# Performance work log

Measured on AMD Instinct MI355X. Metric: run time of the kernel, lower is better.

Reference implementation:

```python
import jax, jax.numpy as jnp
import numpy as np

N = 8192       # num_nodes
DEG = 16       # edges per node
E = N * DEG    # num_edges
F = 128        # num_features
R = 20         # num_rbf_features
L = 3          # num_message_passing_layers
CUT = 3.0      # cutoff_dist


def setup_inputs() -> dict:
    key = jax.random.key(0)
    ks = jax.random.split(key, 18)
    atoms = jax.random.randint(ks[0], (N,), 1, 119)
    # every node appears as a destination exactly DEG times -> bincount > 0
    idx_i = jnp.repeat(jnp.arange(N), DEG)
    idx_j = jax.random.randint(ks[1], (E,), 0, N)
    raw = jax.random.normal(ks[2], (E, 3), jnp.float32)
    rel_dir = raw / jnp.linalg.norm(raw, axis=-1, keepdims=True)
    rel_dist = jax.random.uniform(ks[3], (E,), jnp.float32, 0.1, CUT - 1e-3)
    emb = (jax.random.normal(ks[4], (119, F), jnp.float32) / np.sqrt(F)).at[0].set(0.0)
    def w(k, shape, fan_in):
        return jax.random.normal(k, shape, jnp.float32) / np.sqrt(fan_in)
    return {
        'atoms': atoms, 'idx_i': idx_i, 'idx_j': idx_j,
        'rel_dir': rel_dir, 'rel_dist': rel_dist, 'emb': emb,
        'msg_w1': w(ks[5], (L, F, F), F), 'msg_b1': jnp.zeros((L, F), jnp.float32),
        'msg_w2': w(ks[6], (L, F, 3 * F), F), 'msg_b2': jnp.zeros((L, 3 * F), jnp.float32),
        'rbf_w': w(ks[7], (L, R, 3 * F), R), 'rbf_b': jnp.zeros((L, 3 * F), jnp.float32),
        'Uw': w(ks[8], (L, F, F), F), 'Vw': w(ks[9], (L, F, F), F),
        'upd_w1': w(ks[10], (L, 2 * F, F), 2 * F), 'upd_b1': jnp.zeros((L, F), jnp.float32),
        'upd_w2': w(ks[11], (L, F, 3 * F), F), 'upd_b2': jnp.zeros((L, 3 * F), jnp.float32),
    }


def painn_forward(atoms, idx_i, idx_j, rel_dir, rel_dist, emb,
                  msg_w1, msg_b1, msg_w2, msg_b2, rbf_w, rbf_b,
                  Uw, Vw, upd_w1, upd_b1, upd_w2, upd_b2):
    silu = jax.nn.silu
    # cosine cutoff and sinusoidal RBF features of edge distances
    cut = 0.5 * (jnp.cos(jnp.pi * rel_dist / CUT) + 1.0)               # [E]
    n = jnp.arange(1, R + 1, dtype=rel_dist.dtype)
    rbf = jnp.sin(n * jnp.pi * rel_dist[:, None] / CUT) / rel_dist[:, None]  # [E,R]

    s = emb[atoms]                                   # [N,F]
    v = jnp.zeros((N, F, 3), s.dtype)                # [N,F,3]
    counts = jax.ops.segment_sum(jnp.ones(E, s.dtype), idx_i, num_segments=N)  # bincount

    for l in range(L):
        # ---- message block ----
        phi = silu(s @ msg_w1[l] + msg_b1[l]) @ msg_w2[l] + msg_b2[l]  # [N,3F]
        W = (rbf @ rbf_w[l] + rbf_b[l]) * cut[:, None]                 # [E,3F]
        phi_W = phi[idx_j] * W                                         # [E,3F]
        p_vv, p_ss, p_vs = jnp.split(phi_W, 3, axis=-1)
        ds = jax.ops.segment_sum(p_ss, idx_i, num_segments=N) / counts[:, None]
        ve = v[idx_j] * p_vv[..., None] + p_vs[..., None] * rel_dir[:, None, :]  # [E,F,3]
        dv = jax.ops.segment_sum(ve, idx_i, num_segments=N) / counts[:, None, None]
        s = s + ds
        v = v + dv
        # ---- update block ----
        Uv = jnp.einsum('nfc,fg->ngc', v, Uw[l])       # [N,F,3]
        Vv = jnp.einsum('nfc,fg->ngc', v, Vw[l])       # [N,F,3]
        a_in = jnp.concatenate([jnp.linalg.norm(Vv, axis=-1), s], axis=-1)  # [N,2F]
        a = silu(a_in @ upd_w1[l] + upd_b1[l]) @ upd_w2[l] + upd_b2[l]      # [N,3F]
        a_vv, a_sv, a_ss = jnp.split(a, 3, axis=-1)
        s = s + a_ss + a_sv * jnp.sum(Uv * Vv, axis=-1)
        v = v + Uv * a_vv[..., None]
    return s, v


def reference(atoms, idx_i, idx_j, rel_dir, rel_dist, emb,
              msg_w1, msg_b1, msg_w2, msg_b2, rbf_w, rbf_b,
              Uw, Vw, upd_w1, upd_b1, upd_w2, upd_b2):
    return painn_forward(atoms, idx_i, idx_j, rel_dir, rel_dist, emb,
                         msg_w1, msg_b1, msg_w2, msg_b2, rbf_w, rbf_b,
                         Uw, Vw, upd_w1, upd_b1, upd_w2, upd_b2)
```

## Files before the change

### kernel.cpp

```cpp
#include <hip/hip_runtime.h>
#include <hip/hip_fp16.h>

#define N_NODES 8192
#define DEG     16
#define NEDGE   (N_NODES*DEG)
#define F       128
#define F3      384
#define RBF     20
#define NLAYER  3
#define NF      (N_NODES*F)
#define PI_F    3.14159265358979f

typedef unsigned short u16;
typedef __bf16 bf16x8 __attribute__((ext_vector_type(8)));
typedef float  f32x4  __attribute__((ext_vector_type(4)));
typedef _Float16 f16x2 __attribute__((ext_vector_type(2)));

__device__ __forceinline__ float bf2f(u16 u){ return __uint_as_float(((unsigned)u)<<16); }
__device__ __forceinline__ u16 f2bf(float f){
  unsigned x = __float_as_uint(f);
  unsigned r = (x + 0x7FFFu + ((x>>16)&1u)) >> 16;
  return (u16)r;
}
__device__ __forceinline__ float lo_bf(unsigned u){ return __uint_as_float(u<<16); }
__device__ __forceinline__ float hi_bf(unsigned u){ return __uint_as_float(u & 0xFFFF0000u); }
__device__ __forceinline__ float silu_f(float x){ return x / (1.f + __expf(-x)); }
__device__ __forceinline__ float ldsrc(const void* src, int i, int bf){
  return bf ? bf2f(((const u16*)src)[i]) : ((const float*)src)[i];
}
__device__ __forceinline__ unsigned packh2(float a, float b){
  return (unsigned)__half_as_ushort(__float2half(a)) |
         ((unsigned)__half_as_ushort(__float2half(b)) << 16);
}
__device__ __forceinline__ float fdot2u(unsigned a, unsigned b, float c){
  return __builtin_amdgcn_fdot2(__builtin_bit_cast(f16x2, a),
                                __builtin_bit_cast(f16x2, b), c, false);
}

__global__ void k_detect(const u16* __restrict__ rd, int* __restrict__ flag){
  if (threadIdx.x == 0 && blockIdx.x == 0){
    int ok = 1;
    for (int i = 0; i < 128; i++){
      float v = bf2f(rd[2*i]);
      if (!(v > 0.01f && v < 4.0f)) { ok = 0; break; }
    }
    *flag = ok;
  }
}

__device__ __forceinline__ void splitw(const void* src, u16* bh, u16* bl,
                                       int i, int K, int Ncol, int bf){
  int kn = K*Ncol; int l = i/kn; int r = i - l*kn; int k = r/Ncol; int n = r - k*Ncol;
  float w = ldsrc(src, i, bf);
  u16 h = f2bf(w);
  size_t o = (size_t)l*kn + (size_t)n*K + k;
  bh[o] = h; bl[o] = f2bf(w - bf2f(h));
}

__global__ __launch_bounds__(256) void k_prep(
    const void* mb1, const void* mb2, const void* b1, const void* b2,
    const void* rw,  const void* rb,
    const void* mw1, const void* mw2, const void* w1, const void* w2,
    const void* Uw,  const void* Vw,
    const void* dist, const void* dirv, const int* __restrict__ idxj,
    const int* __restrict__ atoms, const void* __restrict__ emb,
    float* c_mb1, float* c_mb2, float* c_b1, float* c_b2,
    unsigned* rwp2,
    u16* mw1h, u16* mw1l, u16* mw2h, u16* mw2l, u16* w1h, u16* w1l,
    u16* w2h, u16* w2l, u16* uvh, u16* uvl,
    uint4* edata,
    float* s, u16* s_h, u16* s_l,
    u16* p0h, u16* p0l, u16* bufA16, u16* bufB16,
    const int* __restrict__ flag){
  int i = blockIdx.x*256 + threadIdx.x;
  int bf = *flag;
  const int S0=NLAYER*F, S1=NLAYER*F3, S2=NLAYER*F, S3=NLAYER*F3;
  const int S4=NLAYER*11*F3;
  const int S5=NLAYER*F*F, S6=NLAYER*F*F3, S7=NLAYER*2*F*F, S8=NLAYER*F*F3, S9=NLAYER*256*F;
  if (i < S0){ c_mb1[i]=ldsrc(mb1,i,bf); return; } i-=S0;
  if (i < S1){ c_mb2[i]=ldsrc(mb2,i,bf); return; } i-=S1;
  if (i < S2){ c_b1[i] =ldsrc(b1, i,bf); return; } i-=S2;
  if (i < S3){ c_b2[i] =ldsrc(b2, i,bf); return; } i-=S3;
  if (i < S4){
    int l = i/(11*F3); int r = i - l*(11*F3); int r2 = r/F3; int col = r - r2*F3;
    float w0, w1v;
    if (r2 < 10){
      w0  = ldsrc(rw, (l*RBF + 2*r2  )*F3 + col, bf);
      w1v = ldsrc(rw, (l*RBF + 2*r2+1)*F3 + col, bf);
    } else {
      w0  = ldsrc(rb, l*F3 + col, bf);
      w1v = 0.f;
    }
    rwp2[i] = packh2(w0, w1v);
    return;
  } i-=S4;
  if (i < S5){ splitw(mw1, mw1h, mw1l, i, F,   F,  bf); return; } i-=S5;
  if (i < S6){ splitw(mw2, mw2h, mw2l, i, F,   F3, bf); return; } i-=S6;
  if (i < S7){ splitw(w1,  w1h,  w1l,  i, 2*F, F,  bf); return; } i-=S7;
  if (i < S8){ splitw(w2,  w2h,  w2l,  i, F,   F3, bf); return; } i-=S8;
  if (i < S9){
    int l=i/(256*F); int r=i-l*(256*F); int n=r>>7; int k=r&127;
    int si=(l*F+k)*F+(n&127);
    float w = ldsrc((n<128)?Uw:Vw, si, bf);
    u16 h=f2bf(w); uvh[i]=h; uvl[i]=f2bf(w-bf2f(h));
    return;
  } i-=S9;
  if (i < NEDGE){
    int e = i;
    float d = ldsrc(dist, e, bf);
    float th = PI_F*d*(1.f/3.f);
    float c  = __cosf(th);
    float s1 = __sinf(th);
    float cut = 0.5f*(c + 1.0f);
    float ic = cut/d;
    float sk[RBF+1];
    sk[0] = s1; float sm1 = 0.f, s0 = s1;
    #pragma unroll
    for (int k=1;k<=RBF;k++){ float sn = 2.f*c*s0 - sm1; sk[k-1] = s0; sm1 = s0; s0 = sn; }
    unsigned o[16];
    #pragma unroll
    for (int r2=0;r2<10;r2++)
      o[r2] = packh2(sk[2*r2]*ic, sk[2*r2+1]*ic);
    o[10] = packh2(cut, 0.f);
    o[11] = __float_as_uint(ldsrc(dirv, e*3+0, bf));
    o[12] = __float_as_uint(ldsrc(dirv, e*3+1, bf));
    o[13] = __float_as_uint(ldsrc(dirv, e*3+2, bf));
    o[14] = (unsigned)idxj[e];
    o[15] = 0;
    uint4* dst = edata + (size_t)e*4;
    dst[0] = make_uint4(o[0],o[1],o[2],o[3]);
    dst[1] = make_uint4(o[4],o[5],o[6],o[7]);
    dst[2] = make_uint4(o[8],o[9],o[10],o[11]);
    dst[3] = make_uint4(o[12],o[13],o[14],o[15]);
    return;
  } i-=NEDGE;
  if (i < NF){
    int n = i >> 7, f = i & 127;
    float sv = ldsrc(emb, atoms[n]*F + f, bf);
    s[i] = sv;
    u16 hb = f2bf(sv); s_h[i] = hb; s_l[i] = f2bf(sv - bf2f(hb));
    p0h[i]=0; p0h[NF+i]=0; p0h[2*(size_t)NF+i]=0;
    p0l[i]=0; p0l[NF+i]=0; p0l[2*(size_t)NF+i]=0;
    bufA16[(size_t)i*4+2]=0; bufA16[(size_t)i*4+3]=0;
    bufB16[(size_t)i*2+1]=0;
  }
}
#define PREP_TOTAL (NLAYER*(F+F3+F+F3+11*F3+F*F+F*F3+2*F*F+F*F3+256*F) + NEDGE + NF)

__global__ __launch_bounds__(256) void k_msg(const u16* __restrict__ s_h,
                                             const u16* __restrict__ s_l,
                                             const u16* __restrict__ w1h_,
                                             const u16* __restrict__ w1l_,
                                             const u16* __restrict__ w2h_,
                                             const u16* __restrict__ w2l_,
                                             const float* __restrict__ b1,
                                             const float* __restrict__ b2,
                                             u16* __restrict__ bufA16,
                                             u16* __restrict__ bufB16){
  __shared__ u16 Ah[16*136], Al[16*136];
  __shared__ u16 Hh[16*136], Hl[16*136];
  __shared__ u16 Bh[64*136], Bl[64*136];
  int t = threadIdx.x, lane = t&63, w = t>>6;
  int row0 = blockIdx.x<<4;
  int l15 = lane&15, q8 = (lane>>4)<<3, qrow = (lane>>4)<<2;

  #pragma unroll
  for (int q=0;q<2;q++){
    int id = t + 256*q; int pl = id>>8, rem = id&255, r = rem>>4, c = (rem&15)<<3;
    *(uint4*)((pl?Al:Ah)+r*136+c) = *(const uint4*)((pl?s_l:s_h) + (size_t)(row0+r)*F + c);
  }

  for (int cg=0;cg<2;cg++){
    __syncthreads();
    #pragma unroll
    for (int q=0;q<8;q++){
      int id = t + 256*q; int pl = id>>10, rem = id&1023, r = rem>>4, c = (rem&15)<<3;
      *(uint4*)((pl?Bl:Bh)+r*136+c) = *(const uint4*)((pl?w1l_:w1h_) + (size_t)(cg*64+r)*F + c);
    }
    __syncthreads();
    f32x4 acc; acc[0]=0;acc[1]=0;acc[2]=0;acc[3]=0;
// ... 21 lines not shown
  for (int cg=0;cg<6;cg++){
    __syncthreads();
    #pragma unroll
    for (int q=0;q<8;q++){
      int id = t + 256*q; int pl = id>>10, rem = id&1023, r = rem>>4, c = (rem&15)<<3;
      *(uint4*)((pl?Bl:Bh)+r*136+c) = *(const uint4*)((pl?w2l_:w2h_) + (size_t)(cg*64+r)*F + c);
    }
    __syncthreads();
    f32x4 acc; acc[0]=0;acc[1]=0;acc[2]=0;acc[3]=0;
    #pragma unroll
    for (int k0=0;k0<F;k0+=32){
      bf16x8 a_h = *(const bf16x8*)&Hh[l15*136 + k0 + q8];
      bf16x8 a_l = *(const bf16x8*)&Hl[l15*136 + k0 + q8];
      bf16x8 b_h = *(const bf16x8*)&Bh[(w*16+l15)*136 + k0 + q8];
      bf16x8 b_l = *(const bf16x8*)&Bl[(w*16+l15)*136 + k0 + q8];
      acc = __builtin_amdgcn_mfma_f32_16x16x32_bf16(a_h, b_h, acc, 0,0,0);
      acc = __builtin_amdgcn_mfma_f32_16x16x32_bf16(a_h, b_l, acc, 0,0,0);
      acc = __builtin_amdgcn_mfma_f32_16x16x32_bf16(a_l, b_h, acc, 0,0,0);
    }
    int gc = cg*64 + w*16 + l15;
    float bb = b2[gc];
    #pragma unroll
    for (int r=0;r<4;r++){
      int grow = row0 + qrow + r;
      u16 v = f2bf(acc[r] + bb);
      size_t rowo = (size_t)grow*F;
      if (gc < F)        bufA16[(rowo + gc)*4 + 0]     = v;
      else if (gc < 2*F) bufA16[(rowo + gc - F)*4 + 1] = v;
      else               bufB16[(rowo + gc - 2*F)*2]   = v;
    }
  }
}

__global__ __launch_bounds__(256) void k_agg(const uint4* __restrict__ ed_g,
                                             const uint2* __restrict__ bufA,
                                             const unsigned* __restrict__ bufB,
                                             const unsigned* __restrict__ rwp2,
                                             const u16* __restrict__ vi_h,
                                             const u16* __restrict__ vi_l,
                                             u16* __restrict__ vo_h,
                                             u16* __restrict__ vo_l,
                                             float* __restrict__ s,
                                             u16* __restrict__ s_h,
                                             u16* __restrict__ s_l){
  __shared__ uint4 ed4[128];
  int t = threadIdx.x;
  int half = t >> 7, f = t & 127;

  unsigned rw2[3][11];
  #pragma unroll
  for (int r2=0;r2<11;r2++){
    rw2[0][r2] = rwp2[r2*F3 + f];
    rw2[1][r2] = rwp2[r2*F3 + F + f];
    rw2[2][r2] = rwp2[r2*F3 + 2*F + f];
  }

  int nA = blockIdx.x * 2;
  if (t < 128) ed4[t] = ed_g[(size_t)nA*64 + t];
  __syncthreads();

  int n = nA + half;
  int base = half*64;
  float ds=0.f, dv0=0.f, dv1=0.f, dv2=0.f;

  int j0 = (int)(ed4[base+3].z & (N_NODES-1));
  uint2    pa = bufA[(size_t)j0*F + f];
  unsigned pb = bufB[(size_t)j0*F + f];
  for (int el=0;el<DEG;el++){
    uint2 cpa = pa; unsigned cpb = pb;
    if (el+1 < DEG){
      int j1 = (int)(ed4[base+(el+1)*4+3].z & (N_NODES-1));
      pa = bufA[(size_t)j1*F + f];
      pb = bufB[(size_t)j1*F + f];
    }
    uint4 q0 = ed4[base+el*4+0];
    uint4 q1 = ed4[base+el*4+1];
    uint4 q2 = ed4[base+el*4+2];
    uint4 q3 = ed4[base+el*4+3];
    unsigned rc[11] = {q0.x,q0.y,q0.z,q0.w, q1.x,q1.y,q1.z,q1.w, q2.x,q2.y,q2.z};
    float Wvv = 0.f, Wss = 0.f, Wvs = 0.f;
    #pragma unroll
    for (int r2=0;r2<11;r2++){
      Wvv = fdot2u(rc[r2], rw2[0][r2], Wvv);
      Wss = fdot2u(rc[r2], rw2[1][r2], Wss);
      Wvs = fdot2u(rc[r2], rw2[2][r2], Wvs);
    }
    float pvv = Wvv*lo_bf(cpa.x), pss = Wss*hi_bf(cpa.x), pvs = Wvs*lo_bf(cpb);
    ds += pss;
    dv0 += lo_bf(cpa.y)*pvv + pvs*__uint_as_float(q2.w);
    dv1 += hi_bf(cpa.y)*pvv + pvs*__uint_as_float(q3.x);
    dv2 += hi_bf(cpb)  *pvv + pvs*__uint_as_float(q3.y);
  }
  size_t i = (size_t)n*F + f;
  const float inv = 1.f/DEG;
  float sv = s[i] + ds*inv;
  s[i] = sv;
  { u16 hb = f2bf(sv); s_h[i] = hb; s_l[i] = f2bf(sv - bf2f(hb)); }
  float o0 = bf2f(vi_h[i])              + bf2f(vi_l[i])              + dv0*inv;
  float o1 = bf2f(vi_h[NF+i])           + bf2f(vi_l[NF+i])           + dv1*inv;
  float o2 = bf2f(vi_h[2*(size_t)NF+i]) + bf2f(vi_l[2*(size_t)NF+i]) + dv2*inv;
  u16 h0=f2bf(o0), h1=f2bf(o1), h2=f2bf(o2);
  vo_h[i]=h0; vo_h[NF+i]=h1; vo_h[2*(size_t)NF+i]=h2;
  vo_l[i]=f2bf(o0-bf2f(h0)); vo_l[NF+i]=f2bf(o1-bf2f(h1)); vo_l[2*(size_t)NF+i]=f2bf(o2-bf2f(h2));
}

struct Pre4 { uint4 v0, v1, v2, v3; };

__device__ __forceinline__ Pre4 load_tile(int idx, int t,
    const u16* uvh, const u16* uvl,
    const u16* w1h_, const u16* w1l_,
    const u16* w2h_, const u16* w2l_,
    const u16* mw1h_, const u16* mw1l_,
    const u16* mw2h_, const u16* mw2l_){
  const u16 *bh, *bl; int st, off;
  if (idx < 4){       bh=uvh;   bl=uvl;   st=128; off = idx*(64*128); }
  else if (idx < 8){  int r2=idx-4;
                      bh=w1h_;  bl=w1l_;  st=256; off = (r2&1)*(64*256) + (r2>>1)*128; }
  else if (idx < 14){ bh=w2h_;  bl=w2l_;  st=128; off = (idx-8)*(64*128); }
  else if (idx < 16){ bh=mw1h_; bl=mw1l_; st=128; off = (idx-14)*(64*128); }
  else {              bh=mw2h_; bl=mw2l_; st=128; off = (idx-16)*(64*128); }
  Pre4 p;
  { int id=t;      int hl=id>>10, rem=id&1023, r=rem>>4, c8=(rem&15)<<3;
    p.v0 = *(const uint4*)((hl?bl:bh) + (size_t)off + r*st + c8); }
  { int id=t+512;  int hl=id>>10, rem=id&1023, r=rem>>4, c8=(rem&15)<<3;
    p.v1 = *(const uint4*)((hl?bl:bh) + (size_t)off + r*st + c8); }
  { int id=t+1024; int hl=id>>10, rem=id&1023, r=rem>>4, c8=(rem&15)<<3;
    p.v2 = *(const uint4*)((hl?bl:bh) + (size_t)off + r*st + c8); }
  { int id=t+1536; int hl=id>>10, rem=id&1023, r=rem>>4, c8=(rem&15)<<3;
    p.v3 = *(const uint4*)((hl?bl:bh) + (size_t)off + r*st + c8); }
  return p;
}
__device__ __forceinline__ void write_tile(u16* Bt, int t, Pre4 p){
  { int id=t;      int hl=id>>10, rem=id&1023, r=rem>>4, c8=(rem&15)<<3;
    *(uint4*)(Bt + hl*(64*136) + r*136 + c8) = p.v0; }
  { int id=t+512;  int hl=id>>10, rem=id&1023, r=rem>>4, c8=(rem&15)<<3;
    *(uint4*)(Bt + hl*(64*136) + r*136 + c8) = p.v1; }
  { int id=t+1024; int hl=id>>10, rem=id&1023, r=rem>>4, c8=(rem&15)<<3;
    *(uint4*)(Bt + hl*(64*136) + r*136 + c8) = p.v2; }
  { int id=t+1536; int hl=id>>10, rem=id&1023, r=rem>>4, c8=(rem&15)<<3;
    *(uint4*)(Bt + hl*(64*136) + r*136 + c8) = p.v3; }
}
#define TSRC uvh,uvl,w1h_,w1l_,w2h_,w2l_,mw1h_,mw1l_,mw2h_,mw2l_

__global__ __launch_bounds__(512) void k_fused(
    const u16* __restrict__ uvh,  const u16* __restrict__ uvl,
    const u16* __restrict__ w1h_, const u16* __restrict__ w1l_,
    const u16* __restrict__ w2h_, const u16* __restrict__ w2l_,
    const float* __restrict__ b1, const float* __restrict__ b2,
    const u16* __restrict__ mw1h_, const u16* __restrict__ mw1l_,
    const u16* __restrict__ mw2h_, const u16* __restrict__ mw2l_,
    const float* __restrict__ mb1, const float* __restrict__ mb2,
    float* __restrict__ s, u16* __restrict__ s_h, u16* __restrict__ s_l,
    u16* __restrict__ v_h, u16* __restrict__ v_l,
    u16* __restrict__ bufA16, u16* __restrict__ bufB16,
    float* __restrict__ out){
  __shared__ __align__(16) u16 AV [6*32*136];
  __shared__ __align__(16) u16 Bt [2*64*136];
  __shared__ __align__(16) u16 AIb[2*32*264];
  __shared__ __align__(16) u16 Hx [2*32*136];
  int t = threadIdx.x;
  int lane = t&63, w = t>>6;
  int qr = (w>>2)<<4;
  int qw = w&3;
  int l15 = lane&15, q8 = (lane>>4)<<3, qrow = (lane>>4)<<2;
  int row0 = blockIdx.x<<5;
  bool domsg = (mw1h_ != nullptr);
  const int NT = domsg ? 22 : 14;

#define MFMA_STEP(ACC, KS, AH, AL) { \
    bf16x8 _bh = *(const bf16x8*)&Bt[(qw*16+l15)*136 + (KS)*32 + q8]; \
    bf16x8 _bl = *(const bf16x8*)&Bt[64*136 + (qw*16+l15)*136 + (KS)*32 + q8]; \
    ACC = __builtin_amdgcn_mfma_f32_16x16x32_bf16(AH, _bh, ACC, 0,0,0); \
    ACC = __builtin_amdgcn_mfma_f32_16x16x32_bf16(AH, _bl, ACC, 0,0,0); \
    ACC = __builtin_amdgcn_mfma_f32_16x16x32_bf16(AL, _bh, ACC, 0,0,0); }

  #pragma unroll
  for (int q=0;q<6;q++){
    int id = t + 512*q;
    int chl = id>>9, rem = id&511, r = rem>>4, c8 = (rem&15)<<3;
    const u16* src = ((chl&1)? v_l : v_h) + (size_t)(chl>>1)*NF + (size_t)(row0+r)*F + c8;
    *(uint4*)&AV[((size_t)chl*32 + r)*136 + c8] = *(const uint4*)src;
  }
  #pragma unroll
  for (int q=0;q<2;q++){
    int id = t + 512*q;
    int hl = id>>9, rem = id&511, r = rem>>4, c8 = (rem&15)<<3;
    const u16* src = (hl? s_l : s_h) + (size_t)(row0+r)*F + c8;
    *(uint4*)&AIb[(size_t)hl*32*264 + r*264 + 128 + c8] = *(const uint4*)src;
  }

  Pre4 pre = load_tile(0, t, TSRC);

  f32x4 aU[2][3], aV[2][3];
  #pragma unroll
  for (int cg=0; cg<4; cg++){
    __syncthreads();
    write_tile(Bt, t, pre);
    __syncthreads();
    pre = load_tile(cg+1, t, TSRC);
    f32x4 ac0, ac1, ac2;
    ac0[0]=0;ac0[1]=0;ac0[2]=0;ac0[3]=0; ac1=ac0; ac2=ac0;
    #pragma unroll
    for (int k0=0;k0<F;k0+=32){
      bf16x8 b_h = *(const bf16x8*)&Bt[(qw*16+l15)*136 + k0 + q8];
      bf16x8 b_l = *(const bf16x8*)&Bt[64*136 + (qw*16+l15)*136 + k0 + q8];
      {
        bf16x8 a_h = *(const bf16x8*)&AV[(0*32 + qr + l15)*136 + k0 + q8];
        bf16x8 a_l = *(const bf16x8*)&AV[(1*32 + qr + l15)*136 + k0 + q8];
        ac0 = __builtin_amdgcn_mfma_f32_16x16x32_bf16(a_h, b_h, ac0, 0,0,0);
        ac0 = __builtin_amdgcn_mfma_f32_16x16x32_bf16(a_h, b_l, ac0, 0,0,0);
        ac0 = __builtin_amdgcn_mfma_f32_16x16x32_bf16(a_l, b_h, ac0, 0,0,0);
      }
      {
        bf16x8 a_h = *(const bf16x8*)&AV[(2*32 + qr + l15)*136 + k0 + q8];
        bf16x8 a_l = *(const bf16x8*)&AV[(3*32 + qr + l15)*136 + k0 + q8];
        ac1 = __builtin_amdgcn_mfma_f32_16x16x32_bf16(a_h, b_h, ac1, 0,0,0);
        ac1 = __builtin_amdgcn_mfma_f32_16x16x32_bf16(a_h, b_l, ac1, 0,0,0);
        ac1 = __builtin_amdgcn_mfma_f32_16x16x32_bf16(a_l, b_h, ac1, 0,0,0);
      }
      {
        bf16x8 a_h = *(const bf16x8*)&AV[(4*32 + qr + l15)*136 + k0 + q8];
        bf16x8 a_l = *(const bf16x8*)&AV[(5*32 + qr + l15)*136 + k0 + q8];
        ac2 = __builtin_amdgcn_mfma_f32_16x16x32_bf16(a_h, b_h, ac2, 0,0,0);
        ac2 = __builtin_amdgcn_mfma_f32_16x16x32_bf16(a_h, b_l, ac2, 0,0,0);
// ... 79 lines not shown
  bf16x8 ha3l = *(const bf16x8*)&Hx[32*136 + (qr+l15)*136 + 96 + q8];
  __half* aL = (__half*)AIb;
  #pragma unroll
  for (int cg=0; cg<6; cg++){
    __syncthreads();
    write_tile(Bt, t, pre);
    __syncthreads();
    if (9+cg < NT)
      pre = load_tile(9+cg, t, TSRC);
    f32x4 acc; acc[0]=0;acc[1]=0;acc[2]=0;acc[3]=0;
    MFMA_STEP(acc, 0, ha0h, ha0l);
    MFMA_STEP(acc, 1, ha1h, ha1l);
    MFMA_STEP(acc, 2, ha2h, ha2l);
    MFMA_STEP(acc, 3, ha3h, ha3l);
    int gc = cg*64 + qw*16 + l15;
    float bb = b2[gc];
    #pragma unroll
    for (int r=0;r<4;r++)
      aL[(qr+qrow+r)*392 + gc] = __float2half(acc[r] + bb);
  }
  __syncthreads();

  #pragma unroll
  for (int g=0; g<2; g++){
    #pragma unroll
    for (int r=0; r<4; r++){
      int row = qr+qrow+r;
      int col = g*64+qw*16+l15;
      int grow = row0+row;
      size_t i = (size_t)grow*F + col;
      float avv = __half2float(aL[row*392 + col]);
      float asv = __half2float(aL[row*392 + F + col]);
      float ass = __half2float(aL[row*392 + 2*F + col]);
      float sv = s[i] + ass + asv*dotf[g][r];
      s[i] = sv;
      u16 hb = f2bf(sv); u16 lb = f2bf(sv - bf2f(hb));
      s_h[i]=hb; s_l[i]=lb;
      float nv[3];
      #pragma unroll
      for (int c=0;c<3;c++){
        float vold = bf2f(AV[((2*c)*32+row)*136+col]) + bf2f(AV[((2*c+1)*32+row)*136+col]);
        nv[c] = vold + aU[g][c][r]*avv;
      }
      u16 h0=f2bf(nv[0]), h1=f2bf(nv[1]), h2=f2bf(nv[2]);
      v_h[i]=h0; v_h[NF+i]=h1; v_h[2*(size_t)NF+i]=h2;
      v_l[i]=f2bf(nv[0]-bf2f(h0)); v_l[NF+i]=f2bf(nv[1]-bf2f(h1)); v_l[2*(size_t)NF+i]=f2bf(nv[2]-bf2f(h2));
      bufA16[i*4+2]=h0; bufA16[i*4+3]=h1; bufB16[i*2+1]=h2;
      if (out){
        out[i] = sv;
        out[NF + i*3 + 0] = nv[0];
        out[NF + i*3 + 1] = nv[1];
        out[NF + i*3 + 2] = nv[2];
      }
      if (domsg){
        Hx[row*136+col] = hb;
        Hx[32*136 + row*136+col] = lb;
      }
    }
  }

  if (domsg){
    __syncthreads();
    bf16x8 sa0h = *(const bf16x8*)&Hx[(qr+l15)*136 +  0 + q8];
    bf16x8 sa1h = *(const bf16x8*)&Hx[(qr+l15)*136 + 32 + q8];
    bf16x8 sa2h = *(const bf16x8*)&Hx[(qr+l15)*136 + 64 + q8];
    bf16x8 sa3h = *(const bf16x8*)&Hx[(qr+l15)*136 + 96 + q8];
    bf16x8 sa0l = *(const bf16x8*)&Hx[32*136 + (qr+l15)*136 +  0 + q8];
    bf16x8 sa1l = *(const bf16x8*)&Hx[32*136 + (qr+l15)*136 + 32 + q8];
    bf16x8 sa2l = *(const bf16x8*)&Hx[32*136 + (qr+l15)*136 + 64 + q8];
    bf16x8 sa3l = *(const bf16x8*)&Hx[32*136 + (qr+l15)*136 + 96 + q8];
    f32x4 acc4A, acc4B;
    acc4A[0]=0;acc4A[1]=0;acc4A[2]=0;acc4A[3]=0; acc4B=acc4A;
    __syncthreads();
    write_tile(Bt, t, pre);
    __syncthreads();
    pre = load_tile(15, t, TSRC);
    MFMA_STEP(acc4A, 0, sa0h, sa0l);
    MFMA_STEP(acc4A, 1, sa1h, sa1l);
    MFMA_STEP(acc4A, 2, sa2h, sa2l);
    MFMA_STEP(acc4A, 3, sa3h, sa3l);
    __syncthreads();
    write_tile(Bt, t, pre);
    __syncthreads();
    pre = load_tile(16, t, TSRC);
    MFMA_STEP(acc4B, 0, sa0h, sa0l);
    MFMA_STEP(acc4B, 1, sa1h, sa1l);
    MFMA_STEP(acc4B, 2, sa2h, sa2l);
// ... 36 lines not shown
      MFMA_STEP(acc, 2, mh2h, mh2l);
      MFMA_STEP(acc, 3, mh3h, mh3l);
      int gc = cg*64 + qw*16 + l15;
      float bb = mb2[gc];
      #pragma unroll
      for (int r=0;r<4;r++){
        int grow = row0 + qr + qrow + r;
        u16 v16 = f2bf(acc[r] + bb);
        size_t rowo = (size_t)grow*F;
        if (gc < F)        bufA16[(rowo + gc)*4 + 0]     = v16;
        else if (gc < 2*F) bufA16[(rowo + gc - F)*4 + 1] = v16;
        else               bufB16[(rowo + gc - 2*F)*2]   = v16;
      }
    }
  }
#undef MFMA_STEP
}

extern "C" void kernel_launch(void* const* d_in, const int* in_sizes, int n_in,
                              void* d_out, int out_size, void* d_ws, size_t ws_size,
                              hipStream_t stream) {
  const int* atoms   = (const int*)d_in[0];
  const int* idxj    = (const int*)d_in[2];

  float* W = (float*)d_ws;
  size_t off = 64;
  int* flag = (int*)d_ws;
  #define ALLOCF(name, cnt) float* name = W+off; off += (((cnt)+63)&~(size_t)63)
  #define ALLOCU(name, cnt) u16* name = (u16*)(W+off); off += ((((cnt)+1)/2+63)&~(size_t)63)
  ALLOCF(c_mb1, NLAYER*F);
  ALLOCF(c_mb2, NLAYER*F3);
  ALLOCF(c_b1,  NLAYER*F);
  ALLOCF(c_b2,  NLAYER*F3);
  unsigned* c_rwp2 = (unsigned*)(W+off); off += ((NLAYER*11*F3+63)&~(size_t)63);
  uint4* edata = (uint4*)(W+off); off += (size_t)NEDGE*16;
  ALLOCU(w_mw1h, NLAYER*F*F);   ALLOCU(w_mw1l, NLAYER*F*F);
  ALLOCU(w_mw2h, NLAYER*F*F3);  ALLOCU(w_mw2l, NLAYER*F*F3);
  ALLOCU(w_uvh,  NLAYER*256*F); ALLOCU(w_uvl,  NLAYER*256*F);
  ALLOCU(w_w1h,  NLAYER*F*256); ALLOCU(w_w1l,  NLAYER*F*256);
  ALLOCU(w_w2h,  NLAYER*F*F3);  ALLOCU(w_w2l,  NLAYER*F*F3);
  uint2* bufA = (uint2*)(W+off); off += (size_t)2*NF;
  unsigned* bufB = (unsigned*)(W+off); off += (size_t)NF;
  ALLOCU(p0h, (size_t)3*NF); ALLOCU(p0l, (size_t)3*NF);
  ALLOCU(p1h, (size_t)3*NF); ALLOCU(p1l, (size_t)3*NF);
  ALLOCU(s_h,  NF); ALLOCU(s_l,  NF);
  ALLOCF(s,    NF);

  k_detect<<<1, 64, 0, stream>>>((const u16*)d_in[4], flag);
  k_prep<<<(PREP_TOTAL+255)/256, 256, 0, stream>>>(
      d_in[7], d_in[9], d_in[15], d_in[17],
      d_in[10], d_in[11],
      d_in[6], d_in[8], d_in[14], d_in[16],
      d_in[12], d_in[13],
      d_in[4], d_in[3], idxj,
      atoms, d_in[5],
      c_mb1, c_mb2, c_b1, c_b2, c_rwp2,
      w_mw1h, w_mw1l, w_mw2h, w_mw2l, w_w1h, w_w1l,
      w_w2h, w_w2l, w_uvh, w_uvl, edata,
      s, s_h, s_l, p0h, p0l, (u16*)bufA, (u16*)bufB, flag);

  k_msg<<<N_NODES/16, 256, 0, stream>>>(
      s_h, s_l,
      w_mw1h, w_mw1l, w_mw2h, w_mw2l,
      c_mb1, c_mb2,
      (u16*)bufA, (u16*)bufB);

  for (int l=0; l<NLAYER; l++){
    u16* vih = (l & 1) ? p1h : p0h;
    u16* vil = (l & 1) ? p1l : p0l;
    u16* voh = (l & 1) ? p0h : p1h;
    u16* vol = (l & 1) ? p0l : p1l;
    k_agg<<<N_NODES/2, 256, 0, stream>>>(
        edata, bufA, bufB, c_rwp2 + (size_t)l*11*F3,
        vih, vil, voh, vol, s, s_h, s_l);
    int ln = l + 1;
    int domsg = (l < NLAYER-1);
    k_fused<<<N_NODES/32, 512, 0, stream>>>(
        w_uvh + (size_t)l*256*F, w_uvl + (size_t)l*256*F,
        w_w1h + (size_t)l*F*256, w_w1l + (size_t)l*F*256,
        w_w2h + (size_t)l*F*F3,  w_w2l + (size_t)l*F*F3,
        c_b1 + (size_t)l*F, c_b2 + (size_t)l*F3,
        domsg ? w_mw1h + (size_t)ln*F*F  : nullptr,
        domsg ? w_mw1l + (size_t)ln*F*F  : nullptr,
        domsg ? w_mw2h + (size_t)ln*F*F3 : nullptr,
        domsg ? w_mw2l + (size_t)ln*F*F3 : nullptr,
        domsg ? c_mb1 + (size_t)ln*F  : nullptr,
        domsg ? c_mb2 + (size_t)ln*F3 : nullptr,
        s, s_h, s_l, voh, vol,
        (u16*)bufA, (u16*)bufB,
        (l == NLAYER-1) ? (float*)d_out : nullptr);
  }
}
```

Measured before the change: 319.2 us.

## Fuse edge aggregation into the update/message kernel with double-buffered edge features

Removes the separate k_agg launch and performs the per-node edge aggregation at the start of the fused update kernel, keeping updated s and v in shared memory instead of writing them to global memory and reading them back. The bufA/bufB message buffers are double-buffered so the kernel can read the previous layer's messages while writing the next. This also drops the s_h/s_l global round trip and the second v ping-pong buffer. In exchange, the aggregation now runs in only N/32 blocks, with 8 rows handled serially per thread group, so less parallelism covers the gather latency. It also adds a 16KB shared-memory array, which may lower occupancy.

```diff
diff --git a/kernel.cpp b/kernel.cpp
--- a/kernel.cpp
+++ b/kernel.cpp
@@ -233,78 +233,6 @@
   }
 }
 
-__global__ __launch_bounds__(256) void k_agg(const uint4* __restrict__ ed_g,
-                                             const uint2* __restrict__ bufA,
-                                             const unsigned* __restrict__ bufB,
-                                             const unsigned* __restrict__ rwp2,
-                                             const u16* __restrict__ vi_h,
-                                             const u16* __restrict__ vi_l,
-                                             u16* __restrict__ vo_h,
-                                             u16* __restrict__ vo_l,
-                                             float* __restrict__ s,
-                                             u16* __restrict__ s_h,
-                                             u16* __restrict__ s_l){
-  __shared__ uint4 ed4[128];
-  int t = threadIdx.x;
-  int half = t >> 7, f = t & 127;
-
-  unsigned rw2[3][11];
-  #pragma unroll
-  for (int r2=0;r2<11;r2++){
-    rw2[0][r2] = rwp2[r2*F3 + f];
-    rw2[1][r2] = rwp2[r2*F3 + F + f];
-    rw2[2][r2] = rwp2[r2*F3 + 2*F + f];
-  }
-
-  int nA = blockIdx.x * 2;
-  if (t < 128) ed4[t] = ed_g[(size_t)nA*64 + t];
-  __syncthreads();
-
-  int n = nA + half;
-  int base = half*64;
-  float ds=0.f, dv0=0.f, dv1=0.f, dv2=0.f;
-
-  int j0 = (int)(ed4[base+3].z & (N_NODES-1));
-  uint2    pa = bufA[(size_t)j0*F + f];
-  unsigned pb = bufB[(size_t)j0*F + f];
-  for (int el=0;el<DEG;el++){
-    uint2 cpa = pa; unsigned cpb = pb;
-    if (el+1 < DEG){
-      int j1 = (int)(ed4[base+(el+1)*4+3].z & (N_NODES-1));
-      pa = bufA[(size_t)j1*F + f];
-      pb = bufB[(size_t)j1*F + f];
-    }
-    uint4 q0 = ed4[base+el*4+0];
-    uint4 q1 = ed4[base+el*4+1];
-    uint4 q2 = ed4[base+el*4+2];
-    uint4 q3 = ed4[base+el*4+3];
-    unsigned rc[11] = {q0.x,q0.y,q0.z,q0.w, q1.x,q1.y,q1.z,q1.w, q2.x,q2.y,q2.z};
-    float Wvv = 0.f, Wss = 0.f, Wvs = 0.f;
-    #pragma unroll
-    for (int r2=0;r2<11;r2++){
-      Wvv = fdot2u(rc[r2], rw2[0][r2], Wvv);
-      Wss = fdot2u(rc[r2], rw2[1][r2], Wss);
-      Wvs = fdot2u(rc[r2], rw2[2][r2], Wvs);
-    }
-    float pvv = Wvv*lo_bf(cpa.x), pss = Wss*hi_bf(cpa.x), pvs = Wvs*lo_bf(cpb);
-    ds += pss;
-    dv0 += lo_bf(cpa.y)*pvv + pvs*__uint_as_float(q2.w);
-    dv1 += hi_bf(cpa.y)*pvv + pvs*__uint_as_float(q3.x);
-    dv2 += hi_bf(cpb)  *pvv + pvs*__uint_as_float(q3.y);
-  }
-  size_t i = (size_t)n*F + f;
-  const float inv = 1.f/DEG;
-  float sv = s[i] + ds*inv;
-  s[i] = sv;
-  { u16 hb = f2bf(sv); s_h[i] = hb; s_l[i] = f2bf(sv - bf2f(hb)); }
-  float o0 = bf2f(vi_h[i])              + bf2f(vi_l[i])              + dv0*inv;
-  float o1 = bf2f(vi_h[NF+i])           + bf2f(vi_l[NF+i])           + dv1*inv;
-  float o2 = bf2f(vi_h[2*(size_t)NF+i]) + bf2f(vi_l[2*(size_t)NF+i]) + dv2*inv;
-  u16 h0=f2bf(o0), h1=f2bf(o1), h2=f2bf(o2);
-  vo_h[i]=h0; vo_h[NF+i]=h1; vo_h[2*(size_t)NF+i]=h2;
-  vo_l[i]=f2bf(o0-bf2f(h0)); vo_l[NF+i]=f2bf(o1-bf2f(h1)); vo_l[2*(size_t)NF+i]=f2bf(o2-bf2f(h2));
-}
-
 struct Pre4 { uint4 v0, v1, v2, v3; };
 
 __device__ __forceinline__ Pre4 load_tile(int idx, int t,
@@ -343,7 +271,10 @@
 }
 #define TSRC uvh,uvl,w1h_,w1l_,w2h_,w2l_,mw1h_,mw1l_,mw2h_,mw2l_
 
-__global__ __launch_bounds__(512) void k_fused(
+__global__ __launch_bounds__(512) void k_fused2(
+    const uint4* __restrict__ edata,
+    const uint2* __restrict__ rdA, const unsigned* __restrict__ rdB,
+    const unsigned* __restrict__ rwp2,
     const u16* __restrict__ uvh,  const u16* __restrict__ uvl,
     const u16* __restrict__ w1h_, const u16* __restrict__ w1l_,
     const u16* __restrict__ w2h_, const u16* __restrict__ w2l_,
@@ -351,7 +282,7 @@
     const u16* __restrict__ mw1h_, const u16* __restrict__ mw1l_,
     const u16* __restrict__ mw2h_, const u16* __restrict__ mw2l_,
     const float* __restrict__ mb1, const float* __restrict__ mb2,
-    float* __restrict__ s, u16* __restrict__ s_h, u16* __restrict__ s_l,
+    float* __restrict__ s,
     u16* __restrict__ v_h, u16* __restrict__ v_l,
     u16* __restrict__ bufA16, u16* __restrict__ bufB16,
     float* __restrict__ out){
@@ -359,6 +290,7 @@
   __shared__ __align__(16) u16 Bt [2*64*136];
   __shared__ __align__(16) u16 AIb[2*32*264];
   __shared__ __align__(16) u16 Hx [2*32*136];
+  __shared__ float sS[32*128];
   int t = threadIdx.x;
   int lane = t&63, w = t>>6;
   int qr = (w>>2)<<4;
@@ -382,15 +314,73 @@
     const u16* src = ((chl&1)? v_l : v_h) + (size_t)(chl>>1)*NF + (size_t)(row0+r)*F + c8;
     *(uint4*)&AV[((size_t)chl*32 + r)*136 + c8] = *(const uint4*)src;
   }
+
+  int f = t & 127;
+  int slotU = __builtin_amdgcn_readfirstlane(t >> 7);
+  unsigned rw2[3][11];
   #pragma unroll
-  for (int q=0;q<2;q++){
-    int id = t + 512*q;
-    int hl = id>>9, rem = id&511, r = rem>>4, c8 = (rem&15)<<3;
-    const u16* src = (hl? s_l : s_h) + (size_t)(row0+r)*F + c8;
-    *(uint4*)&AIb[(size_t)hl*32*264 + r*264 + 128 + c8] = *(const uint4*)src;
-  }
+  for (int r2=0;r2<11;r2++){
+    rw2[0][r2] = rwp2[r2*F3 + f];
+    rw2[1][r2] = rwp2[r2*F3 + F + f];
+    rw2[2][r2] = rwp2[r2*F3 + 2*F + f];
+  }
+  const uint4* __restrict__ ed = edata + (size_t)(row0 + slotU*8)*64;
 
   Pre4 pre = load_tile(0, t, TSRC);
+
+  __syncthreads();
+
+  {
+    const float inv = 1.f/DEG;
+    int j0 = (int)(ed[3].z & (N_NODES-1));
+    uint2    pa = rdA[(size_t)j0*F + f];
+    unsigned pb = rdB[(size_t)j0*F + f];
+    for (int ns=0; ns<8; ns++){
+      int row = slotU*8 + ns;
+      float ds=0.f, dv0=0.f, dv1=0.f, dv2=0.f;
+      #pragma unroll
+      for (int el=0; el<16; el++){
+        uint2 cpa = pa; unsigned cpb = pb;
+        if (!(el==15 && ns==7)){
+          int nns = (el==15) ? ns+1 : ns;
+          int nel = (el==15) ? 0 : el+1;
+          int j1 = (int)(ed[nns*64 + nel*4 + 3].z & (N_NODES-1));
+          pa = rdA[(size_t)j1*F + f];
+          pb = rdB[(size_t)j1*F + f];
+        }
+        uint4 q0 = ed[ns*64 + el*4 + 0];
+        uint4 q1 = ed[ns*64 + el*4 + 1];
+        uint4 q2 = ed[ns*64 + el*4 + 2];
+        uint4 q3 = ed[ns*64 + el*4 + 3];
+        unsigned rc[11] = {q0.x,q0.y,q0.z,q0.w, q1.x,q1.y,q1.z,q1.w, q2.x,q2.y,q2.z};
+        float Wvv = 0.f, Wss = 0.f, Wvs = 0.f;
+        #pragma unroll
+        for (int r2=0;r2<11;r2++){
+          Wvv = fdot2u(rc[r2], rw2[0][r2], Wvv);
+          Wss = fdot2u(rc[r2], rw2[1][r2], Wss);
+          Wvs = fdot2u(rc[r2], rw2[2][r2], Wvs);
+        }
+        float pvv = Wvv*lo_bf(cpa.x), pss = Wss*hi_bf(cpa.x), pvs = Wvs*lo_bf(cpb);
+        ds += pss;
+        dv0 += lo_bf(cpa.y)*pvv + pvs*__uint_as_float(q2.w);
+        dv1 += hi_bf(cpa.y)*pvv + pvs*__uint_as_float(q3.x);
+        dv2 += hi_bf(cpb)  *pvv + pvs*__uint_as_float(q3.y);
+      }
+      size_t i = (size_t)(row0+row)*F + f;
+      float sv = s[i] + ds*inv;
+      sS[row*128 + f] = sv;
+      u16 sh = f2bf(sv);
+      AIb[row*264 + 128 + f] = sh;
+      AIb[32*264 + row*264 + 128 + f] = f2bf(sv - bf2f(sh));
+      float o0 = bf2f(AV[(0*32+row)*136+f]) + bf2f(AV[(1*32+row)*136+f]) + dv0*inv;
+      float o1 = bf2f(AV[(2*32+row)*136+f]) + bf2f(AV[(3*32+row)*136+f]) + dv1*inv;
+      float o2 = bf2f(AV[(4*32+row)*136+f]) + bf2f(AV[(5*32+row)*136+f]) + dv2*inv;
+      u16 h0=f2bf(o0), h1=f2bf(o1), h2=f2bf(o2);
+      AV[(0*32+row)*136+f]=h0; AV[(1*32+row)*136+f]=f2bf(o0-bf2f(h0));
+      AV[(2*32+row)*136+f]=h1; AV[(3*32+row)*136+f]=f2bf(o1-bf2f(h1));
+      AV[(4*32+row)*136+f]=h2; AV[(5*32+row)*136+f]=f2bf(o2-bf2f(h2));
+    }
+  }
 
   f32x4 aU[2][3], aV[2][3];
   #pragma unroll
@@ -536,10 +526,9 @@
       float avv = __half2float(aL[row*392 + col]);
       float asv = __half2float(aL[row*392 + F + col]);
       float ass = __half2float(aL[row*392 + 2*F + col]);
-      float sv = s[i] + ass + asv*dotf[g][r];
+      float sv = sS[row*128 + col] + ass + asv*dotf[g][r];
       s[i] = sv;
       u16 hb = f2bf(sv); u16 lb = f2bf(sv - bf2f(hb));
-      s_h[i]=hb; s_l[i]=lb;
       float nv[3];
       #pragma unroll
       for (int c=0;c<3;c++){
@@ -549,7 +538,6 @@
       u16 h0=f2bf(nv[0]), h1=f2bf(nv[1]), h2=f2bf(nv[2]);
       v_h[i]=h0; v_h[NF+i]=h1; v_h[2*(size_t)NF+i]=h2;
       v_l[i]=f2bf(nv[0]-bf2f(h0)); v_l[NF+i]=f2bf(nv[1]-bf2f(h1)); v_l[2*(size_t)NF+i]=f2bf(nv[2]-bf2f(h2));
-      bufA16[i*4+2]=h0; bufA16[i*4+3]=h1; bufB16[i*2+1]=h2;
       if (out){
         out[i] = sv;
         out[NF + i*3 + 0] = nv[0];
@@ -557,6 +545,7 @@
         out[NF + i*3 + 2] = nv[2];
       }
       if (domsg){
+        bufA16[i*4+2]=h0; bufA16[i*4+3]=h1; bufB16[i*2+1]=h2;
         Hx[row*136+col] = hb;
         Hx[32*136 + row*136+col] = lb;
       }
@@ -666,10 +655,11 @@
   ALLOCU(w_uvh,  NLAYER*256*F); ALLOCU(w_uvl,  NLAYER*256*F);
   ALLOCU(w_w1h,  NLAYER*F*256); ALLOCU(w_w1l,  NLAYER*F*256);
   ALLOCU(w_w2h,  NLAYER*F*F3);  ALLOCU(w_w2l,  NLAYER*F*F3);
-  uint2* bufA = (uint2*)(W+off); off += (size_t)2*NF;
-  unsigned* bufB = (unsigned*)(W+off); off += (size_t)NF;
+  uint2* bufA0 = (uint2*)(W+off); off += (size_t)2*NF;
+  unsigned* bufB0 = (unsigned*)(W+off); off += (size_t)NF;
+  uint2* bufA1 = (uint2*)(W+off); off += (size_t)2*NF;
+  unsigned* bufB1 = (unsigned*)(W+off); off += (size_t)NF;
   ALLOCU(p0h, (size_t)3*NF); ALLOCU(p0l, (size_t)3*NF);
-  ALLOCU(p1h, (size_t)3*NF); ALLOCU(p1l, (size_t)3*NF);
   ALLOCU(s_h,  NF); ALLOCU(s_l,  NF);
   ALLOCF(s,    NF);
 
@@ -684,25 +674,23 @@
       c_mb1, c_mb2, c_b1, c_b2, c_rwp2,
       w_mw1h, w_mw1l, w_mw2h, w_mw2l, w_w1h, w_w1l,
       w_w2h, w_w2l, w_uvh, w_uvl, edata,
-      s, s_h, s_l, p0h, p0l, (u16*)bufA, (u16*)bufB, flag);
+      s, s_h, s_l, p0h, p0l, (u16*)bufA0, (u16*)bufB0, flag);
 
   k_msg<<<N_NODES/16, 256, 0, stream>>>(
       s_h, s_l,
       w_mw1h, w_mw1l, w_mw2h, w_mw2l,
       c_mb1, c_mb2,
-      (u16*)bufA, (u16*)bufB);
+      (u16*)bufA0, (u16*)bufB0);
 
   for (int l=0; l<NLAYER; l++){
-    u16* vih = (l & 1) ? p1h : p0h;
-    u16* vil = (l & 1) ? p1l : p0l;
-    u16* voh = (l & 1) ? p0h : p1h;
-    u16* vol = (l & 1) ? p0l : p1l;
-    k_agg<<<N_NODES/2, 256, 0, stream>>>(
-        edata, bufA, bufB, c_rwp2 + (size_t)l*11*F3,
-        vih, vil, voh, vol, s, s_h, s_l);
+    const uint2*    rdA = (l & 1) ? bufA1 : bufA0;
+    const unsigned* rdB = (l & 1) ? bufB1 : bufB0;
+    u16* wrA = (u16*)((l & 1) ? bufA0 : bufA1);
+    u16* wrB = (u16*)((l & 1) ? bufB0 : bufB1);
     int ln = l + 1;
     int domsg = (l < NLAYER-1);
-    k_fused<<<N_NODES/32, 512, 0, stream>>>(
+    k_fused2<<<N_NODES/32, 512, 0, stream>>>(
+        edata, rdA, rdB, c_rwp2 + (size_t)l*11*F3,
         w_uvh + (size_t)l*256*F, w_uvl + (size_t)l*256*F,
         w_w1h + (size_t)l*F*256, w_w1l + (size_t)l*F*256,
         w_w2h + (size_t)l*F*F3,  w_w2l + (size_t)l*F*F3,
@@ -713,8 +701,8 @@
         domsg ? w_mw2l + (size_t)ln*F*F3 : nullptr,
         domsg ? c_mb1 + (size_t)ln*F  : nullptr,
         domsg ? c_mb2 + (size_t)ln*F3 : nullptr,
-        s, s_h, s_l, voh, vol,
-        (u16*)bufA, (u16*)bufB,
+        s, p0h, p0l,
+        wrA, wrB,
         (l == NLAYER-1) ? (float*)d_out : nullptr);
   }
 }
```

New measurement: 403.6 us. +26.4%, slower.

## Compute per-edge RBF filter weights with f16 MFMA in aggregation kernel

Applied to the files above, without the earlier changes.

The per-edge RBF-to-filter projection in the aggregation kernel used to be done with scalar fdot2 loops in registers. It is now a small f16 MFMA that writes a 32x384 weight tile into LDS. Edge data is split so that direction and neighbour index sit in a separate aux array. The transposed RBF weights are swizzled in LDS, and neighbour feature gathers are prefetched four deep instead of one. In exchange, each block stages a large LDS footprint (weights plus the WL tile), which may reduce occupancy, and the per-block weight load is repeated across 4096 blocks.

```diff
diff --git a/kernel.cpp b/kernel.cpp
--- a/kernel.cpp
+++ b/kernel.cpp
@@ -13,6 +13,7 @@
 
 typedef unsigned short u16;
 typedef __bf16 bf16x8 __attribute__((ext_vector_type(8)));
+typedef _Float16 f16x8 __attribute__((ext_vector_type(8)));
 typedef float  f32x4  __attribute__((ext_vector_type(4)));
 typedef _Float16 f16x2 __attribute__((ext_vector_type(2)));
 
@@ -31,10 +32,6 @@
 __device__ __forceinline__ unsigned packh2(float a, float b){
   return (unsigned)__half_as_ushort(__float2half(a)) |
          ((unsigned)__half_as_ushort(__float2half(b)) << 16);
-}
-__device__ __forceinline__ float fdot2u(unsigned a, unsigned b, float c){
-  return __builtin_amdgcn_fdot2(__builtin_bit_cast(f16x2, a),
-                                __builtin_bit_cast(f16x2, b), c, false);
 }
 
 __global__ void k_detect(const u16* __restrict__ rd, int* __restrict__ flag){
@@ -65,33 +62,33 @@
     const void* dist, const void* dirv, const int* __restrict__ idxj,
     const int* __restrict__ atoms, const void* __restrict__ emb,
     float* c_mb1, float* c_mb2, float* c_b1, float* c_b2,
-    unsigned* rwp2,
+    unsigned* rwT,
     u16* mw1h, u16* mw1l, u16* mw2h, u16* mw2l, u16* w1h, u16* w1l,
     u16* w2h, u16* w2l, u16* uvh, u16* uvl,
     uint4* edata,
+    uint4* eaux,
     float* s, u16* s_h, u16* s_l,
     u16* p0h, u16* p0l, u16* bufA16, u16* bufB16,
     const int* __restrict__ flag){
   int i = blockIdx.x*256 + threadIdx.x;
   int bf = *flag;
   const int S0=NLAYER*F, S1=NLAYER*F3, S2=NLAYER*F, S3=NLAYER*F3;
-  const int S4=NLAYER*11*F3;
+  const int S4=NLAYER*384*16;
   const int S5=NLAYER*F*F, S6=NLAYER*F*F3, S7=NLAYER*2*F*F, S8=NLAYER*F*F3, S9=NLAYER*256*F;
   if (i < S0){ c_mb1[i]=ldsrc(mb1,i,bf); return; } i-=S0;
   if (i < S1){ c_mb2[i]=ldsrc(mb2,i,bf); return; } i-=S1;
   if (i < S2){ c_b1[i] =ldsrc(b1, i,bf); return; } i-=S2;
   if (i < S3){ c_b2[i] =ldsrc(b2, i,bf); return; } i-=S3;
   if (i < S4){
-    int l = i/(11*F3); int r = i - l*(11*F3); int r2 = r/F3; int col = r - r2*F3;
-    float w0, w1v;
+    int l = i/(384*16); int r = i - l*(384*16); int col = r>>4; int r2 = r&15;
+    float w0 = 0.f, w1v = 0.f;
     if (r2 < 10){
       w0  = ldsrc(rw, (l*RBF + 2*r2  )*F3 + col, bf);
       w1v = ldsrc(rw, (l*RBF + 2*r2+1)*F3 + col, bf);
-    } else {
+    } else if (r2 == 10){
       w0  = ldsrc(rb, l*F3 + col, bf);
-      w1v = 0.f;
-    }
-    rwp2[i] = packh2(w0, w1v);
+    }
+    rwT[i] = packh2(w0, w1v);
     return;
   } i-=S4;
   if (i < S5){ splitw(mw1, mw1h, mw1l, i, F,   F,  bf); return; } i-=S5;
@@ -117,21 +114,21 @@
     sk[0] = s1; float sm1 = 0.f, s0 = s1;
     #pragma unroll
     for (int k=1;k<=RBF;k++){ float sn = 2.f*c*s0 - sm1; sk[k-1] = s0; sm1 = s0; s0 = sn; }
-    unsigned o[16];
+    unsigned o[11];
     #pragma unroll
     for (int r2=0;r2<10;r2++)
       o[r2] = packh2(sk[2*r2]*ic, sk[2*r2+1]*ic);
     o[10] = packh2(cut, 0.f);
-    o[11] = __float_as_uint(ldsrc(dirv, e*3+0, bf));
-    o[12] = __float_as_uint(ldsrc(dirv, e*3+1, bf));
-    o[13] = __float_as_uint(ldsrc(dirv, e*3+2, bf));
-    o[14] = (unsigned)idxj[e];
-    o[15] = 0;
     uint4* dst = edata + (size_t)e*4;
     dst[0] = make_uint4(o[0],o[1],o[2],o[3]);
     dst[1] = make_uint4(o[4],o[5],o[6],o[7]);
-    dst[2] = make_uint4(o[8],o[9],o[10],o[11]);
-    dst[3] = make_uint4(o[12],o[13],o[14],o[15]);
+    dst[2] = make_uint4(o[8],o[9],o[10],0u);
+    dst[3] = make_uint4(0u,0u,0u,0u);
+    eaux[e] = make_uint4(
+        __float_as_uint(ldsrc(dirv, e*3+0, bf)),
+        __float_as_uint(ldsrc(dirv, e*3+1, bf)),
+        __float_as_uint(ldsrc(dirv, e*3+2, bf)),
+        (unsigned)idxj[e]);
     return;
   } i-=NEDGE;
   if (i < NF){
@@ -145,7 +142,7 @@
     bufB16[(size_t)i*2+1]=0;
   }
 }
-#define PREP_TOTAL (NLAYER*(F+F3+F+F3+11*F3+F*F+F*F3+2*F*F+F*F3+256*F) + NEDGE + NF)
+#define PREP_TOTAL (NLAYER*(F+F3+F+F3+384*16+F*F+F*F3+2*F*F+F*F3+256*F) + NEDGE + NF)
 
 __global__ __launch_bounds__(256) void k_msg(const u16* __restrict__ s_h,
                                              const u16* __restrict__ s_l,
@@ -233,64 +230,86 @@
   }
 }
 
-__global__ __launch_bounds__(256) void k_agg(const uint4* __restrict__ ed_g,
-                                             const uint2* __restrict__ bufA,
-                                             const unsigned* __restrict__ bufB,
-                                             const unsigned* __restrict__ rwp2,
-                                             const u16* __restrict__ vi_h,
-                                             const u16* __restrict__ vi_l,
-                                             u16* __restrict__ vo_h,
-                                             u16* __restrict__ vo_l,
-                                             float* __restrict__ s,
-                                             u16* __restrict__ s_h,
-                                             u16* __restrict__ s_l){
-  __shared__ uint4 ed4[128];
+__global__ __launch_bounds__(256) void k_agg2(const uint4* __restrict__ ed_g,
+                                              const uint4* __restrict__ aux_g,
+                                              const uint2* __restrict__ bufA,
+                                              const unsigned* __restrict__ bufB,
+                                              const unsigned* __restrict__ rwT,
+                                              const u16* __restrict__ vi_h,
+                                              const u16* __restrict__ vi_l,
+                                              u16* __restrict__ vo_h,
+                                              u16* __restrict__ vo_l,
+                                              float* __restrict__ s,
+                                              u16* __restrict__ s_h,
+                                              u16* __restrict__ s_l){
+  __shared__ __align__(16) uint4 ed4[32*5];
+  __shared__ uint4 aux[32];
+  __shared__ __align__(16) unsigned BT[384*16];
+  __shared__ float WL[32*388];
   int t = threadIdx.x;
+  int nA = blockIdx.x*2;
+  int e0 = nA*DEG;
+
+  if (t < 128){ int e = t>>2, c = t&3; ed4[e*5+c] = ed_g[(size_t)(e0+e)*4 + c]; }
+  if (t < 32) aux[t] = aux_g[e0 + t];
+  #pragma unroll
+  for (int q=0;q<24;q++){
+    int i = t + 256*q;
+    int col = i>>4, r2 = i&15;
+    int wi = (((r2>>2) ^ ((col>>2)&3))<<2) | (r2&3);
+    BT[col*16 + wi] = rwT[i];
+  }
+  __syncthreads();
+
+  {
+    int lane = t&63, w = t>>6;
+    int mt = w&1, ng = w>>1;
+    int l15 = lane&15, ch = lane>>4;
+    f16x8 afr = *(const f16x8*)&ed4[(mt*16 + l15)*5 + ch];
+    #pragma unroll
+    for (int nt=0; nt<12; nt++){
+      int n0 = ng*12 + nt;
+      int col = n0*16 + l15;
+      int wi = (ch ^ ((col>>2)&3))<<2;
+      f16x8 bfr = *(const f16x8*)&BT[col*16 + wi];
+      f32x4 acc; acc[0]=0;acc[1]=0;acc[2]=0;acc[3]=0;
+      acc = __builtin_amdgcn_mfma_f32_16x16x32_f16(afr, bfr, acc, 0,0,0);
+      #pragma unroll
+      for (int r=0;r<4;r++)
+        WL[(mt*16 + (ch<<2) + r)*388 + col] = acc[r];
+    }
+  }
+  __syncthreads();
+
   int half = t >> 7, f = t & 127;
-
-  unsigned rw2[3][11];
-  #pragma unroll
-  for (int r2=0;r2<11;r2++){
-    rw2[0][r2] = rwp2[r2*F3 + f];
-    rw2[1][r2] = rwp2[r2*F3 + F + f];
-    rw2[2][r2] = rwp2[r2*F3 + 2*F + f];
-  }
-
-  int nA = blockIdx.x * 2;
-  if (t < 128) ed4[t] = ed_g[(size_t)nA*64 + t];
-  __syncthreads();
-
   int n = nA + half;
-  int base = half*64;
+  int base = half*16;
   float ds=0.f, dv0=0.f, dv1=0.f, dv2=0.f;
 
-  int j0 = (int)(ed4[base+3].z & (N_NODES-1));
-  uint2    pa = bufA[(size_t)j0*F + f];
-  unsigned pb = bufB[(size_t)j0*F + f];
-  for (int el=0;el<DEG;el++){
-    uint2 cpa = pa; unsigned cpb = pb;
-    if (el+1 < DEG){
-      int j1 = (int)(ed4[base+(el+1)*4+3].z & (N_NODES-1));
-      pa = bufA[(size_t)j1*F + f];
-      pb = bufB[(size_t)j1*F + f];
-    }
-    uint4 q0 = ed4[base+el*4+0];
-    uint4 q1 = ed4[base+el*4+1];
-    uint4 q2 = ed4[base+el*4+2];
-    uint4 q3 = ed4[base+el*4+3];
-    unsigned rc[11] = {q0.x,q0.y,q0.z,q0.w, q1.x,q1.y,q1.z,q1.w, q2.x,q2.y,q2.z};
-    float Wvv = 0.f, Wss = 0.f, Wvs = 0.f;
-    #pragma unroll
-    for (int r2=0;r2<11;r2++){
-      Wvv = fdot2u(rc[r2], rw2[0][r2], Wvv);
-      Wss = fdot2u(rc[r2], rw2[1][r2], Wss);
-      Wvs = fdot2u(rc[r2], rw2[2][r2], Wvs);
-    }
+  uint2 pa[4]; unsigned pb[4];
+  #pragma unroll
+  for (int k=0;k<4;k++){
+    int j = (int)(aux[base+k].w & (N_NODES-1));
+    pa[k] = bufA[(size_t)j*F + f];
+    pb[k] = bufB[(size_t)j*F + f];
+  }
+  #pragma unroll
+  for (int el=0; el<16; el++){
+    uint2 cpa = pa[el&3]; unsigned cpb = pb[el&3];
+    if (el+4 < 16){
+      int j = (int)(aux[base+el+4].w & (N_NODES-1));
+      pa[el&3] = bufA[(size_t)j*F + f];
+      pb[el&3] = bufB[(size_t)j*F + f];
+    }
+    int e = base + el;
+    float Wvv = WL[e*388 + f];
+    float Wss = WL[e*388 + F + f];
+    float Wvs = WL[e*388 + 2*F + f];
     float pvv = Wvv*lo_bf(cpa.x), pss = Wss*hi_bf(cpa.x), pvs = Wvs*lo_bf(cpb);
     ds += pss;
-    dv0 += lo_bf(cpa.y)*pvv + pvs*__uint_as_float(q2.w);
-    dv1 += hi_bf(cpa.y)*pvv + pvs*__uint_as_float(q3.x);
-    dv2 += hi_bf(cpb)  *pvv + pvs*__uint_as_float(q3.y);
+    dv0 += lo_bf(cpa.y)*pvv + pvs*__uint_as_float(aux[e].x);
+    dv1 += hi_bf(cpa.y)*pvv + pvs*__uint_as_float(aux[e].y);
+    dv2 += hi_bf(cpb)  *pvv + pvs*__uint_as_float(aux[e].z);
   }
   size_t i = (size_t)n*F + f;
   const float inv = 1.f/DEG;
@@ -659,8 +678,9 @@
   ALLOCF(c_mb2, NLAYER*F3);
   ALLOCF(c_b1,  NLAYER*F);
   ALLOCF(c_b2,  NLAYER*F3);
-  unsigned* c_rwp2 = (unsigned*)(W+off); off += ((NLAYER*11*F3+63)&~(size_t)63);
+  unsigned* rwT = (unsigned*)(W+off); off += ((NLAYER*384*16+63)&~(size_t)63);
   uint4* edata = (uint4*)(W+off); off += (size_t)NEDGE*16;
+  uint4* eaux  = (uint4*)(W+off); off += (size_t)NEDGE*4;
   ALLOCU(w_mw1h, NLAYER*F*F);   ALLOCU(w_mw1l, NLAYER*F*F);
   ALLOCU(w_mw2h, NLAYER*F*F3);  ALLOCU(w_mw2l, NLAYER*F*F3);
   ALLOCU(w_uvh,  NLAYER*256*F); ALLOCU(w_uvl,  NLAYER*256*F);
@@ -681,9 +701,9 @@
       d_in[12], d_in[13],
       d_in[4], d_in[3], idxj,
       atoms, d_in[5],
-      c_mb1, c_mb2, c_b1, c_b2, c_rwp2,
+      c_mb1, c_mb2, c_b1, c_b2, rwT,
       w_mw1h, w_mw1l, w_mw2h, w_mw2l, w_w1h, w_w1l,
-      w_w2h, w_w2l, w_uvh, w_uvl, edata,
+      w_w2h, w_w2l, w_uvh, w_uvl, edata, eaux,
       s, s_h, s_l, p0h, p0l, (u16*)bufA, (u16*)bufB, flag);
 
   k_msg<<<N_NODES/16, 256, 0, stream>>>(
@@ -697,8 +717,8 @@
     u16* vil = (l & 1) ? p1l : p0l;
     u16* voh = (l & 1) ? p0h : p1h;
     u16* vol = (l & 1) ? p0l : p1l;
-    k_agg<<<N_NODES/2, 256, 0, stream>>>(
-        edata, bufA, bufB, c_rwp2 + (size_t)l*11*F3,
+    k_agg2<<<N_NODES/2, 256, 0, stream>>>(
+        edata, eaux, bufA, bufB, rwT + (size_t)l*384*16,
         vih, vil, voh, vol, s, s_h, s_l);
     int ln = l + 1;
     int domsg = (l < NLAYER-1);
```

Result: slower. 345.3 us (+8.2%).
